# Kernel tuning notes

Hardware: AMD Instinct MI355X
Metric: run time of the kernel (lower is better)

The kernel has to match this reference:

```python
import jax, jax.numpy as jnp
import numpy as np

R_TBR = 0.5
P_BASE = 50.0
ALPHA = 100.0
H_BASELINE = 0.0
T_AMBIENT = -10.0
EPS = 1e-8


def _ternary_quantize(weight):
    gamma = jnp.mean(jnp.abs(weight))
    # round-half-to-even matches torch.round
    return jnp.clip(jnp.round(weight / (gamma + EPS)), -1.0, 1.0)


def _entropy_3bin(w_q):
    n = w_q.size
    # histc(bins=3, min=-1, max=1) on values in {-1,0,1} -> exact bin counts
    counts = jnp.stack([
        jnp.sum(w_q == -1.0),
        jnp.sum(w_q == 0.0),
        jnp.sum(w_q == 1.0),
    ]).astype(jnp.float32)
    p = counts / n
    # -sum p*log2 p over p>0 (jnp.where keeps it jit-safe)
    return -jnp.sum(jnp.where(p > 0, p * jnp.log2(jnp.where(p > 0, p, 1.0)), 0.0))


def setup_inputs() -> dict:
    key = jax.random.key(0)
    k1, k2 = jax.random.split(key)
    x = jax.random.normal(k1, (8192, 4096), dtype=jnp.float32)
    weight = jax.random.normal(k2, (4096, 4096), dtype=jnp.float32)  # [out, in]
    return {"x": x, "weight": weight}


def reference(x, weight):
    w_q = _ternary_quantize(weight)            # ternary {-1,0,1}, shape [out, in]
    entropy = _entropy_3bin(w_q)
    heat_flux = ALPHA * jax.nn.relu(entropy - H_BASELINE)
    q_total = P_BASE + heat_flux
    t_current = T_AMBIENT + q_total * R_TBR    # guardrail value (no overload at T_ambient=-10)
    output = x @ w_q.T                         # F.linear(x, W_q), [N, out]
    return (output, t_current, entropy)
```

## Files before the change

kernel.cpp:

```cpp
#include <hip/hip_runtime.h>
#include <stdint.h>

typedef short bf16x8 __attribute__((ext_vector_type(8)));
typedef float f32x4 __attribute__((ext_vector_type(4)));

#define M_ROWS 8192
#define N_OUT  4096
#define K_DIM  4096
#define NW     16777216.0

__device__ __forceinline__ void gload16(const void* g, void* l) {
    __builtin_amdgcn_global_load_lds((const __attribute__((address_space(1))) void*)g,
                                     (__attribute__((address_space(3))) void*)l,
                                     16, 0, 0);
}

__device__ __forceinline__ unsigned short f2bf(float f) {
    unsigned u = __float_as_uint(f);
    unsigned r = 0x7FFFu + ((u >> 16) & 1u);
    return (unsigned short)((u + r) >> 16);
}

__global__ __launch_bounds__(256) void k_gamma(const float* __restrict__ w,
                                               double* __restrict__ sum) {
    const int n4 = (K_DIM * N_OUT) / 4;
    int idx = blockIdx.x * blockDim.x + threadIdx.x;
    int stride = gridDim.x * blockDim.x;
    const float4* w4 = (const float4*)w;
    double local = 0.0;
    for (int i = idx; i < n4; i += stride) {
        float4 v = w4[i];
        local += (double)fabsf(v.x) + (double)fabsf(v.y) +
                 (double)fabsf(v.z) + (double)fabsf(v.w);
    }
    __shared__ double sm[256];
    sm[threadIdx.x] = local;
    __syncthreads();
    for (int s = 128; s > 0; s >>= 1) {
        if (threadIdx.x < s) sm[threadIdx.x] += sm[threadIdx.x + s];
        __syncthreads();
    }
    if (threadIdx.x == 0) atomicAdd(sum, sm[0]);
}

__global__ __launch_bounds__(256) void k_quant(const float* __restrict__ w,
                                               const double* __restrict__ sum,
                                               unsigned short* __restrict__ wq,
                                               unsigned int* __restrict__ counts,
                                               int do_store) {
    const float gamma = (float)(*sum / NW);
    const float denom = gamma + 1e-8f;
    const int n4 = (K_DIM * N_OUT) / 4;
    int idx = blockIdx.x * blockDim.x + threadIdx.x;
    int stride = gridDim.x * blockDim.x;
    const float4* w4 = (const float4*)w;
    unsigned cm = 0, cp = 0;
    for (int i = idx; i < n4; i += stride) {
        float4 v = w4[i];
        float q0 = fminf(1.f, fmaxf(-1.f, rintf(v.x / denom)));
        float q1 = fminf(1.f, fmaxf(-1.f, rintf(v.y / denom)));
        float q2 = fminf(1.f, fmaxf(-1.f, rintf(v.z / denom)));
        float q3 = fminf(1.f, fmaxf(-1.f, rintf(v.w / denom)));
        cm += (q0 < -0.5f) + (q1 < -0.5f) + (q2 < -0.5f) + (q3 < -0.5f);
        cp += (q0 >  0.5f) + (q1 >  0.5f) + (q2 >  0.5f) + (q3 >  0.5f);
        if (do_store) {
            unsigned b0 = (q0 < -0.5f) ? 0xBF80u : (q0 > 0.5f ? 0x3F80u : 0u);
            unsigned b1 = (q1 < -0.5f) ? 0xBF80u : (q1 > 0.5f ? 0x3F80u : 0u);
            unsigned b2 = (q2 < -0.5f) ? 0xBF80u : (q2 > 0.5f ? 0x3F80u : 0u);
            unsigned b3 = (q3 < -0.5f) ? 0xBF80u : (q3 > 0.5f ? 0x3F80u : 0u);
            uint2 pk;
            pk.x = b0 | (b1 << 16);
            pk.y = b2 | (b3 << 16);
            ((uint2*)wq)[i] = pk;
        }
    }
    __shared__ unsigned smc[512];
    smc[threadIdx.x] = cm;
    smc[256 + threadIdx.x] = cp;
    __syncthreads();
    for (int s = 128; s > 0; s >>= 1) {
        if (threadIdx.x < s) {
            smc[threadIdx.x] += smc[threadIdx.x + s];
            smc[256 + threadIdx.x] += smc[256 + threadIdx.x + s];
        }
        __syncthreads();
    }
    if (threadIdx.x == 0) {
        atomicAdd(&counts[0], smc[0]);
        atomicAdd(&counts[1], smc[256]);
    }
}

__global__ __launch_bounds__(256) void k_cvt(const float* __restrict__ x,
                                             unsigned short* __restrict__ xb) {
    const int n4 = (M_ROWS * K_DIM) / 4;
    int idx = blockIdx.x * blockDim.x + threadIdx.x;
    int stride = gridDim.x * blockDim.x;
    const float4* x4 = (const float4*)x;
    for (int i = idx; i < n4; i += stride) {
        float4 v = x4[i];
        uint2 pk;
        pk.x = (unsigned)f2bf(v.x) | ((unsigned)f2bf(v.y) << 16);
        pk.y = (unsigned)f2bf(v.z) | ((unsigned)f2bf(v.w) << 16);
        ((uint2*)xb)[i] = pk;
    }
}

__global__ void k_fin(const unsigned int* __restrict__ counts,
                      float* __restrict__ outs) {
    double n = NW;
    double c1 = (double)counts[0];
    double c2 = (double)counts[1];
    double c0 = n - c1 - c2;
    double H = 0.0;
    if (c1 > 0.0) { double p = c1 / n; H -= p * log2(p); }
    if (c0 > 0.0) { double p = c0 / n; H -= p * log2(p); }
    if (c2 > 0.0) { double p = c2 / n; H -= p * log2(p); }
    float Hf = (float)H;
    float heat = 100.0f * fmaxf(Hf, 0.0f);
    outs[0] = -10.0f + (50.0f + heat) * 0.5f;
    outs[1] = Hf;
}


__device__ __forceinline__ void stage_half(const unsigned short* __restrict__ A,
                                           const unsigned short* __restrict__ B,
                                           char* lds, int H, int tm, int tn,
                                           int tid, int scol) {
    const int kt = H >> 2;
    const int q  = H & 3;
    const unsigned short* src = (q & 2) ? B : A;
    int rb = ((q & 2) ? tn : tm) * 256 + (q & 1) * 128;
    const unsigned short* g0 = src + (size_t)(rb + (tid >> 3)) * K_DIM + kt * 64 + scol;
    char* d = lds + ((size_t)(kt & 1) << 16) + ((q & 2) << 14) + ((q & 1) << 14) + tid * 16;
    gload16(g0, d);
    gload16(g0 + (size_t)64 * K_DIM, d + 8192);
}

#define MFMA_QUAD(ACCM, ACCN, AF, BF)                                          \
    __builtin_amdgcn_s_barrier();                                              \
    asm volatile("s_waitcnt lgkmcnt(0)" ::: "memory");                         \
    __builtin_amdgcn_s_setprio(1);                                             \
    _Pragma("unroll") for (int mm = 0; mm < 4; ++mm)                           \
    _Pragma("unroll") for (int nn = 0; nn < 2; ++nn)                           \
    _Pragma("unroll") for (int ks = 0; ks < 2; ++ks)                           \
        acc[(ACCM) + mm][(ACCN) + nn] = __builtin_amdgcn_mfma_f32_16x16x32_bf16( \
            AF[mm][ks], BF[nn][ks], acc[(ACCM) + mm][(ACCN) + nn], 0, 0, 0);   \
    __builtin_amdgcn_s_setprio(0);

__global__ __launch_bounds__(512, 2) void k_gemm2(const unsigned short* __restrict__ A,
                                                  const unsigned short* __restrict__ B,
                                                  float* __restrict__ C) {
    extern __shared__ char smem[];
    const int tid  = threadIdx.x;
    const int lane = tid & 63;
    const int wid  = tid >> 6;
    const int wr   = wid >> 2;
    const int wc   = wid & 3;
    const int fr   = lane & 15;
    const int khi  = lane >> 4;

    const int lin = blockIdx.x;
    const int s   = (lin & 7) * 64 + (lin >> 3);
    const int tm  = s & 31;
    const int tn  = s >> 5;

    const int scol = ((tid & 7) * 8) ^ (((tid >> 3) & 1) << 5);
    const int rx = (fr & 1) << 6;

    f32x4 acc[8][4] = {};

    for (int H = 0; H < 5; ++H) stage_half(A, B, smem, H, tm, tn, tid, scol);
    asm volatile("s_waitcnt vmcnt(2)" ::: "memory");
    __builtin_amdgcn_s_barrier();

    bf16x8 afr[4][2], b0[2][2], b1[2][2];

    for (int tau = 0; tau < 64; ++tau) {
        char* abase = smem + ((size_t)(tau & 1) << 16) + ((size_t)wr << 14);
        char* bbase = smem + ((size_t)(tau & 1) << 16) + 32768 + ((size_t)(wc >> 1) << 14);
        const int brow0 = (wc & 1) * 64;
        const int g = tau * 4;

#pragma unroll
        for (int mm = 0; mm < 4; ++mm)
#pragma unroll
            for (int ks = 0; ks < 2; ++ks)
                afr[mm][ks] = *(const bf16x8*)(abase + ((mm * 16 + fr) * 128 + ((ks * 64) ^ rx) + khi * 16));
#pragma unroll
        for (int nn = 0; nn < 2; ++nn)
#pragma unroll
            for (int ks = 0; ks < 2; ++ks)
                b0[nn][ks] = *(const bf16x8*)(bbase + ((brow0 + nn * 16 + fr) * 128 + ((ks * 64) ^ rx) + khi * 16));
        if (g + 5 < 256) stage_half(A, B, smem, g + 5, tm, tn, tid, scol);
        MFMA_QUAD(0, 0, afr, b0)
        __builtin_amdgcn_s_barrier();

#pragma unroll
        for (int nn = 0; nn < 2; ++nn)
#pragma unroll
            for (int ks = 0; ks < 2; ++ks)
                b1[nn][ks] = *(const bf16x8*)(bbase + ((brow0 + 32 + nn * 16 + fr) * 128 + ((ks * 64) ^ rx) + khi * 16));
        if (g + 6 < 256) stage_half(A, B, smem, g + 6, tm, tn, tid, scol);
        MFMA_QUAD(0, 2, afr, b1)
        __builtin_amdgcn_s_barrier();

#pragma unroll
        for (int mm = 0; mm < 4; ++mm)
#pragma unroll
            for (int ks = 0; ks < 2; ++ks)
                afr[mm][ks] = *(const bf16x8*)(abase + ((64 + mm * 16 + fr) * 128 + ((ks * 64) ^ rx) + khi * 16));
        if (g + 7 < 256) stage_half(A, B, smem, g + 7, tm, tn, tid, scol);
        MFMA_QUAD(4, 2, afr, b1)
        __builtin_amdgcn_s_barrier();

        if (g + 8 < 256) stage_half(A, B, smem, g + 8, tm, tn, tid, scol);
        MFMA_QUAD(4, 0, afr, b0)
        if (tau < 62) {
            asm volatile("s_waitcnt vmcnt(2)" ::: "memory");
        } else {
            asm volatile("s_waitcnt vmcnt(0)" ::: "memory");
        }
        __builtin_amdgcn_s_barrier();
    }

    const size_t crow = (size_t)(tm * 256 + wr * 128 + khi * 4);
    const int    ccol = tn * 256 + wc * 64 + fr;
#pragma unroll
    for (int m = 0; m < 8; ++m)
#pragma unroll
        for (int n = 0; n < 4; ++n) {
            float* cp = C + (crow + m * 16) * N_OUT + (ccol + n * 16);
#pragma unroll
            for (int j = 0; j < 4; ++j)
                cp[(size_t)j * N_OUT] = acc[m][n][j];
        }
}

__global__ __launch_bounds__(256) void fb_gemm(const float* __restrict__ X,
                                               const float* __restrict__ W,
                                               const double* __restrict__ sum,
                                               float* __restrict__ C) {
    __shared__ float Xs[64][33];
    __shared__ float Ws[64][33];
    const float gamma = (float)(*sum / NW);
    const float denom = gamma + 1e-8f;
    const int tid = threadIdx.x;
    const int bm = blockIdx.y * 64;
    const int bn = blockIdx.x * 64;
    const int tr = tid >> 4, tc = tid & 15;
    const int lrow = tid >> 2;
    const int lcol = (tid & 3) * 8;
    float acc[4][4] = {};
    for (int k0 = 0; k0 < K_DIM; k0 += 32) {
        const float4* xs = (const float4*)(X + (size_t)(bm + lrow) * K_DIM + k0 + lcol);
        float4 v0 = xs[0], v1 = xs[1];
        Xs[lrow][lcol + 0] = v0.x; Xs[lrow][lcol + 1] = v0.y;
        Xs[lrow][lcol + 2] = v0.z; Xs[lrow][lcol + 3] = v0.w;
        Xs[lrow][lcol + 4] = v1.x; Xs[lrow][lcol + 5] = v1.y;
        Xs[lrow][lcol + 6] = v1.z; Xs[lrow][lcol + 7] = v1.w;
        const float4* wsrc = (const float4*)(W + (size_t)(bn + lrow) * K_DIM + k0 + lcol);
        float4 w0 = wsrc[0], w1 = wsrc[1];
        Ws[lrow][lcol + 0] = fminf(1.f, fmaxf(-1.f, rintf(w0.x / denom)));
        Ws[lrow][lcol + 1] = fminf(1.f, fmaxf(-1.f, rintf(w0.y / denom)));
        Ws[lrow][lcol + 2] = fminf(1.f, fmaxf(-1.f, rintf(w0.z / denom)));
        Ws[lrow][lcol + 3] = fminf(1.f, fmaxf(-1.f, rintf(w0.w / denom)));
        Ws[lrow][lcol + 4] = fminf(1.f, fmaxf(-1.f, rintf(w1.x / denom)));
        Ws[lrow][lcol + 5] = fminf(1.f, fmaxf(-1.f, rintf(w1.y / denom)));
        Ws[lrow][lcol + 6] = fminf(1.f, fmaxf(-1.f, rintf(w1.z / denom)));
        Ws[lrow][lcol + 7] = fminf(1.f, fmaxf(-1.f, rintf(w1.w / denom)));
        __syncthreads();
#pragma unroll 8
        for (int kk = 0; kk < 32; ++kk) {
            float a0 = Xs[tr * 4 + 0][kk], a1 = Xs[tr * 4 + 1][kk];
            float a2 = Xs[tr * 4 + 2][kk], a3 = Xs[tr * 4 + 3][kk];
            float b0 = Ws[tc * 4 + 0][kk], b1 = Ws[tc * 4 + 1][kk];
            float b2 = Ws[tc * 4 + 2][kk], b3 = Ws[tc * 4 + 3][kk];
            acc[0][0] += a0 * b0; acc[0][1] += a0 * b1; acc[0][2] += a0 * b2; acc[0][3] += a0 * b3;
            acc[1][0] += a1 * b0; acc[1][1] += a1 * b1; acc[1][2] += a1 * b2; acc[1][3] += a1 * b3;
            acc[2][0] += a2 * b0; acc[2][1] += a2 * b1; acc[2][2] += a2 * b2; acc[2][3] += a2 * b3;
            acc[3][0] += a3 * b0; acc[3][1] += a3 * b1; acc[3][2] += a3 * b2; acc[3][3] += a3 * b3;
        }
        __syncthreads();
    }
#pragma unroll
    for (int i = 0; i < 4; ++i)
#pragma unroll
        for (int j = 0; j < 4; ++j)
            C[(size_t)(bm + tr * 4 + i) * N_OUT + (bn + tc * 4 + j)] = acc[i][j];
}

extern "C" void kernel_launch(void* const* d_in, const int* in_sizes, int n_in,
                              void* d_out, int out_size, void* d_ws, size_t ws_size,
                              hipStream_t stream) {
    (void)in_sizes; (void)n_in; (void)out_size;
    const float* x = (const float*)d_in[0];
    const float* w = (const float*)d_in[1];
    float* out = (float*)d_out;
    float* scalars = out + (size_t)M_ROWS * N_OUT;

    double* sum = (double*)d_ws;
    unsigned int* counts = (unsigned int*)((char*)d_ws + 8);
    unsigned short* xb = (unsigned short*)((char*)d_ws + 64);
    unsigned short* wq = (unsigned short*)((char*)d_ws + 64 + (size_t)M_ROWS * K_DIM * 2);

    const size_t need = 64 + (size_t)M_ROWS * K_DIM * 2 + (size_t)N_OUT * K_DIM * 2;
    const int fast = (ws_size >= need);

    hipMemsetAsync(d_ws, 0, 16, stream);
    k_gamma<<<1024, 256, 0, stream>>>(w, sum);

    if (fast) {
        k_cvt<<<2048, 256, 0, stream>>>(x, xb);
        k_quant<<<1024, 256, 0, stream>>>(w, sum, wq, counts, 1);
        k_fin<<<1, 1, 0, stream>>>(counts, scalars);
        hipFuncSetAttribute(reinterpret_cast<const void*>(k_gemm2),
                            hipFuncAttributeMaxDynamicSharedMemorySize, 131072);
        k_gemm2<<<dim3(512), 512, 131072, stream>>>(xb, wq, out);
    } else {
        k_quant<<<1024, 256, 0, stream>>>(w, sum, nullptr, counts, 0);
        k_fin<<<1, 1, 0, stream>>>(counts, scalars);
        dim3 grid(N_OUT / 64, M_ROWS / 64);
        fb_gemm<<<grid, 256, 0, stream>>>(x, w, sum, out);
    }
}
```

Baseline: 424.7 us.

## Store GEMM tiles in MFMA fragment order in LDS and reorder staging

Changes the global-to-LDS staging so each 16-byte chunk lands at the position a lane reads for its MFMA fragment. LDS fragment reads become linear lane*16 offsets and the XOR swizzle arithmetic goes away. The prefetch order is also rescheduled: four halves of the next k-tile are issued early and a pair two tiles ahead later, with the wait count raised to allow more loads in flight. The risk is that the global loads become less coalesced, since each lane reads a different row, and that the new ordering may contain buffer hazards.

```diff
diff --git a/kernel.cpp b/kernel.cpp
--- a/kernel.cpp
+++ b/kernel.cpp
@@ -126,15 +126,16 @@
 __device__ __forceinline__ void stage_half(const unsigned short* __restrict__ A,
                                            const unsigned short* __restrict__ B,
                                            char* lds, int H, int tm, int tn,
-                                           int tid, int scol) {
+                                           int tid) {
     const int kt = H >> 2;
     const int q  = H & 3;
     const unsigned short* src = (q & 2) ? B : A;
-    int rb = ((q & 2) ? tn : tm) * 256 + (q & 1) * 128;
-    const unsigned short* g0 = src + (size_t)(rb + (tid >> 3)) * K_DIM + kt * 64 + scol;
-    char* d = lds + ((size_t)(kt & 1) << 16) + ((q & 2) << 14) + ((q & 1) << 14) + tid * 16;
+    const int rb = ((q & 2) ? tn : tm) * 256 + (q & 1) * 128;
+    const int row = rb + ((tid >> 6) << 4) + (tid & 15);
+    const unsigned short* g0 = src + (size_t)row * K_DIM + kt * 64 + ((tid >> 4) & 3) * 8;
+    char* d = lds + ((size_t)(kt & 1) << 16) + (q << 14) + tid * 16;
     gload16(g0, d);
-    gload16(g0 + (size_t)64 * K_DIM, d + 8192);
+    gload16(g0 + 32, d + 8192);
 }
 
 #define MFMA_QUAD(ACCM, ACCN, AF, BF)                                          \
@@ -165,34 +166,37 @@
     const int tm  = s & 31;
     const int tn  = s >> 5;
 
-    const int scol = ((tid & 7) * 8) ^ (((tid >> 3) & 1) << 5);
-    const int rx = (fr & 1) << 6;
-
     f32x4 acc[8][4] = {};
 
-    for (int H = 0; H < 5; ++H) stage_half(A, B, smem, H, tm, tn, tid, scol);
-    asm volatile("s_waitcnt vmcnt(2)" ::: "memory");
+    stage_half(A, B, smem, 0, tm, tn, tid);
+    stage_half(A, B, smem, 1, tm, tn, tid);
+    stage_half(A, B, smem, 2, tm, tn, tid);
+    stage_half(A, B, smem, 3, tm, tn, tid);
+    stage_half(A, B, smem, 6, tm, tn, tid);
+    stage_half(A, B, smem, 7, tm, tn, tid);
+    asm volatile("s_waitcnt vmcnt(0)" ::: "memory");
     __builtin_amdgcn_s_barrier();
 
     bf16x8 afr[4][2], b0[2][2], b1[2][2];
+    const int bsel = (wc & 1) * 4;
 
     for (int tau = 0; tau < 64; ++tau) {
-        char* abase = smem + ((size_t)(tau & 1) << 16) + ((size_t)wr << 14);
-        char* bbase = smem + ((size_t)(tau & 1) << 16) + 32768 + ((size_t)(wc >> 1) << 14);
-        const int brow0 = (wc & 1) * 64;
+        const char* aptr = smem + ((size_t)(tau & 1) << 16) + ((size_t)wr << 14) + lane * 16;
+        const char* bptr = smem + ((size_t)(tau & 1) << 16) + 32768 + ((size_t)(wc >> 1) << 14)
+                         + bsel * 1024 + lane * 16;
         const int g = tau * 4;
 
 #pragma unroll
         for (int mm = 0; mm < 4; ++mm)
 #pragma unroll
             for (int ks = 0; ks < 2; ++ks)
-                afr[mm][ks] = *(const bf16x8*)(abase + ((mm * 16 + fr) * 128 + ((ks * 64) ^ rx) + khi * 16));
+                afr[mm][ks] = *(const bf16x8*)(aptr + (ks * 8 + mm) * 1024);
 #pragma unroll
         for (int nn = 0; nn < 2; ++nn)
 #pragma unroll
             for (int ks = 0; ks < 2; ++ks)
-                b0[nn][ks] = *(const bf16x8*)(bbase + ((brow0 + nn * 16 + fr) * 128 + ((ks * 64) ^ rx) + khi * 16));
-        if (g + 5 < 256) stage_half(A, B, smem, g + 5, tm, tn, tid, scol);
+                b0[nn][ks] = *(const bf16x8*)(bptr + (ks * 8 + nn) * 1024);
+        if (g + 4 < 256) stage_half(A, B, smem, g + 4, tm, tn, tid);
         MFMA_QUAD(0, 0, afr, b0)
         __builtin_amdgcn_s_barrier();
 
@@ -200,8 +204,8 @@
         for (int nn = 0; nn < 2; ++nn)
 #pragma unroll
             for (int ks = 0; ks < 2; ++ks)
-                b1[nn][ks] = *(const bf16x8*)(bbase + ((brow0 + 32 + nn * 16 + fr) * 128 + ((ks * 64) ^ rx) + khi * 16));
-        if (g + 6 < 256) stage_half(A, B, smem, g + 6, tm, tn, tid, scol);
+                b1[nn][ks] = *(const bf16x8*)(bptr + (ks * 8 + 2 + nn) * 1024);
+        if (g + 5 < 256) stage_half(A, B, smem, g + 5, tm, tn, tid);
         MFMA_QUAD(0, 2, afr, b1)
         __builtin_amdgcn_s_barrier();
 
@@ -209,15 +213,15 @@
         for (int mm = 0; mm < 4; ++mm)
 #pragma unroll
             for (int ks = 0; ks < 2; ++ks)
-                afr[mm][ks] = *(const bf16x8*)(abase + ((64 + mm * 16 + fr) * 128 + ((ks * 64) ^ rx) + khi * 16));
-        if (g + 7 < 256) stage_half(A, B, smem, g + 7, tm, tn, tid, scol);
+                afr[mm][ks] = *(const bf16x8*)(aptr + (ks * 8 + 4 + mm) * 1024);
+        if (g + 10 < 256) stage_half(A, B, smem, g + 10, tm, tn, tid);
         MFMA_QUAD(4, 2, afr, b1)
         __builtin_amdgcn_s_barrier();
 
-        if (g + 8 < 256) stage_half(A, B, smem, g + 8, tm, tn, tid, scol);
+        if (g + 11 < 256) stage_half(A, B, smem, g + 11, tm, tn, tid);
         MFMA_QUAD(4, 0, afr, b0)
         if (tau < 62) {
-            asm volatile("s_waitcnt vmcnt(2)" ::: "memory");
+            asm volatile("s_waitcnt vmcnt(4)" ::: "memory");
         } else {
             asm volatile("s_waitcnt vmcnt(0)" ::: "memory");
         }
```

After: 370.4 us. 1.15x faster.
